# Performance work log

Measured on AMD Instinct MI355X. Metric: run time of the kernel, lower is better.

The kernel has to match this reference:

```python
import jax, jax.numpy as jnp
import numpy as np

NUM_CLASSES = 80
STRIDES = (8, 16, 32)
INPUT_SIZE = 640
DIST_THRESH_SQ = 64.0 * 64.0  # assignment uses euclidean dist < 64; compare squared


def make_anchors(input_size):
    pts = []
    for s in STRIDES:
        n = input_size // s
        yv, xv = np.meshgrid(np.arange(n), np.arange(n), indexing='ij')
        g = np.stack([xv, yv], -1).reshape(-1, 2).astype(np.float32) * s + s // 2
        pts.append(g)
    return jnp.asarray(np.concatenate(pts, 0))  # [A, 2]


def bce_logits(x, t):
    # BCEWithLogits, elementwise: -(t*log_sigmoid(x) + (1-t)*log_sigmoid(-x))
    return -(t * jax.nn.log_sigmoid(x) + (1.0 - t) * jax.nn.log_sigmoid(-x))


def iou_loss(pred_boxes, target_boxes):
    # pred: (cx, cy, log_w, log_h); target: (cx, cy, w, h) in pixels
    pc = pred_boxes[:, :2]
    ps = jnp.exp(pred_boxes[:, 2:4])
    p1 = pc - ps / 2.0
    p2 = pc + ps / 2.0
    t1 = target_boxes[:, :2] - target_boxes[:, 2:4] / 2.0
    t2 = target_boxes[:, :2] + target_boxes[:, 2:4] / 2.0
    i1 = jnp.maximum(p1, t1)
    i2 = jnp.minimum(p2, t2)
    inter = jnp.clip(i2[:, 0] - i1[:, 0], 0.0) * jnp.clip(i2[:, 1] - i1[:, 1], 0.0)
    pa = (p2[:, 0] - p1[:, 0]) * (p2[:, 1] - p1[:, 1])
    ta = (t2[:, 0] - t1[:, 0]) * (t2[:, 1] - t1[:, 1])
    union = pa + ta - inter
    return 1.0 - inter / (union + 1e-06)


def setup_inputs() -> dict:
    key = jax.random.key(0)
    k1, k2, k3, k4, k5 = jax.random.split(key, 5)
    B, M = 64, 50
    A = sum((INPUT_SIZE // s) ** 2 for s in STRIDES)  # 8400
    predictions = jax.random.normal(k1, (B, A, 5 + NUM_CLASSES), dtype=jnp.float32)
    cls = jax.random.randint(k2, (B, M), 0, NUM_CLASSES).astype(jnp.float32)
    valid = jax.random.uniform(k3, (B, M)) < 0.6
    cls = jnp.where(valid, cls, -1.0)
    centers = jax.random.uniform(k4, (B, M, 2), minval=0.05, maxval=0.95)
    wh = jax.random.uniform(k5, (B, M, 2), minval=0.02, maxval=0.3)
    targets = jnp.concatenate([cls[..., None], centers, wh], axis=-1).astype(jnp.float32)
    return {"predictions": predictions, "targets": targets, "input_size": 640}


def _per_image(pred, tgt, anchors, num_classes, input_size):
    # pred: [A, 5+C], tgt: [M, 5]
    valid = tgt[:, 0] >= 0.0                              # [M]
    gt_cls = tgt[:, 0].astype(jnp.int32)                  # [M]
    gt_boxes = tgt[:, 1:5] * input_size                   # [M, 4] pixels
    diff = gt_boxes[:, None, :2] - anchors[None, :, :]    # [M, A, 2]
    d2 = jnp.sum(diff * diff, axis=-1)                    # [M, A] squared dist
    d2 = jnp.where(valid[:, None], d2, jnp.inf)
    matched = jnp.argmin(d2, axis=0)                      # [A]
    min_d2 = jnp.min(d2, axis=0)                          # [A]
    pos = min_d2 < DIST_THRESH_SQ                         # [A]
    posf = pos.astype(pred.dtype)
    num_pos = posf.sum()

    obj_loss = bce_logits(pred[:, 4], posf).mean()

    cls_t = jax.nn.one_hot(gt_cls[matched], num_classes, dtype=pred.dtype)  # [A, C]
    cls_bce = bce_logits(pred[:, 5:], cls_t)                                # [A, C]
    denom = jnp.maximum(num_pos, 1.0)
    cls_loss = jnp.where(num_pos > 0,
                         (cls_bce * posf[:, None]).sum() / (denom * num_classes), 0.0)

    iou_l = iou_loss(pred[:, :4], gt_boxes[matched])      # [A]
    box_loss = jnp.where(num_pos > 0, (iou_l * posf).sum() / denom, 0.0)
    return obj_loss, cls_loss, box_loss, num_pos


def reference(predictions, targets, input_size):
    anchors = make_anchors(int(input_size))               # [A, 2]
    fsize = jnp.float32(input_size)
    obj, cls, box, npos = jax.vmap(
        lambda p, t: _per_image(p, t, anchors, NUM_CLASSES, fsize)
    )(predictions, targets)
    obj_loss = obj.sum()
    cls_loss = cls.sum()
    box_loss = box.sum()
    num_fg = npos.sum()
    total = 5.0 * box_loss + obj_loss + cls_loss
    return total, box_loss, obj_loss, cls_loss, num_fg
```

## Files before the change

kernel.cpp:

```cpp
#include <hip/hip_runtime.h>
#include <math.h>

#define NUM_CLASSES 80
#define MT 50
#define ATOT 8400
#define CH 85
#define BLOCK 256
#define CHUNK 256
#define NBY 33

__device__ __forceinline__ float softplus_fast(float x) {
    return fmaxf(x, 0.0f) + __logf(1.0f + __expf(-fabsf(x)));
}

__global__ void zero_acc_kernel(float* acc, int n) {
    int i = blockIdx.x * blockDim.x + threadIdx.x;
    if (i < n) acc[i] = 0.0f;
}

__global__ __launch_bounds__(BLOCK) void yolox_fused(
        const float* __restrict__ pred,
        const float* __restrict__ tgt,
        const int*   __restrict__ isz,
        float* __restrict__ acc) {
    const int b  = blockIdx.y;
    const int by = blockIdx.x;
    const int a0 = by * CHUNK;
    const int nanch = min(CHUNK, ATOT - a0);

    __shared__ float  raw[MT * 5];
    __shared__ float2 sxy[MT];
    __shared__ float2 swh[MT];
    __shared__ float  scls[MT];
    __shared__ int    snv;
    __shared__ int    smask[CHUNK];

    for (int i = threadIdx.x; i < MT * 5; i += BLOCK)
        raw[i] = tgt[(size_t)b * MT * 5 + i];
    __syncthreads();
    if (threadIdx.x == 0) {
        const float fsize = (float)(*isz);
        int nv = 0;
        for (int m = 0; m < MT; ++m) {
            const float c = raw[m * 5 + 0];
            if (c >= 0.0f) {
                sxy[nv]  = make_float2(raw[m * 5 + 1] * fsize, raw[m * 5 + 2] * fsize);
                swh[nv]  = make_float2(raw[m * 5 + 3] * fsize, raw[m * 5 + 4] * fsize);
                scls[nv] = c;
                ++nv;
            }
        }
        snv = nv;
    }
    __syncthreads();
    const int nv = snv;

    float box_s = 0.f, np_s = 0.f;
    smask[threadIdx.x] = -1;

    const int a = a0 + threadIdx.x;
    if (threadIdx.x < nanch) {
        int s, n, idx;
        if (a < 6400)      { s = 8;  n = 80; idx = a; }
        else if (a < 8000) { s = 16; n = 40; idx = a - 6400; }
        else               { s = 32; n = 20; idx = a - 8000; }
        const int yy = idx / n;
        const int xx = idx - yy * n;
        const float ax = (float)(xx * s + (s >> 1));
        const float ay = (float)(yy * s + (s >> 1));

        float best = INFINITY;
        int bestm = 0;
        for (int m = 0; m < nv; ++m) {
            const float2 g = sxy[m];
            const float dx = g.x - ax, dy = g.y - ay;
            const float d2 = dx * dx + dy * dy;
            if (d2 < best) { best = d2; bestm = m; }
        }
        const bool pos = best < 4096.0f;

        if (pos) {
            smask[threadIdx.x] = (int)scls[bestm];
            np_s = 1.0f;
            const float* p = pred + ((size_t)b * ATOT + (size_t)a) * CH;
            const float pcx = p[0], pcy = p[1];
            const float pw = __expf(p[2]), ph = __expf(p[3]);
            const float2 g  = sxy[bestm];
            const float2 wh = swh[bestm];
            const float p1x = pcx - pw * 0.5f, p2x = pcx + pw * 0.5f;
            const float p1y = pcy - ph * 0.5f, p2y = pcy + ph * 0.5f;
            const float t1x = g.x - wh.x * 0.5f, t2x = g.x + wh.x * 0.5f;
            const float t1y = g.y - wh.y * 0.5f, t2y = g.y + wh.y * 0.5f;
            const float iw = fminf(p2x, t2x) - fmaxf(p1x, t1x);
            const float ih = fminf(p2y, t2y) - fmaxf(p1y, t1y);
            const float inter = fmaxf(iw, 0.f) * fmaxf(ih, 0.f);
            const float pa = (p2x - p1x) * (p2y - p1y);
            const float ta = (t2x - t1x) * (t2y - t1y);
            const float uni = pa + ta - inter;
            box_s = 1.0f - inter / (uni + 1e-6f);
        }
    }
    __syncthreads();

    float obj_s = 0.f, cls_s = 0.f;
    const float* base = pred + ((size_t)b * ATOT + (size_t)a0) * CH;
    const int ngroups = (nanch * CH) >> 2;

    for (int g = threadIdx.x; g < ngroups; g += BLOCK) {
        const int le0 = g << 2;
        const unsigned la = __umulhi((unsigned)le0, 3233857729u) >> 6;
        const int c0 = le0 - (int)la * CH;
        const int m0 = smask[la];
        const bool need = (c0 >= 1 && c0 <= 4) || (m0 >= 0 && c0 >= 2);
        if (need) {
            const float4 x4 = *(const float4*)(base + le0);
            const float xs[4] = {x4.x, x4.y, x4.z, x4.w};
            #pragma unroll
            for (int j = 0; j < 4; ++j) {
                const int c = c0 + j;
                if (c == 4) {
                    obj_s += softplus_fast(xs[j]) - (m0 >= 0 ? xs[j] : 0.0f);
                } else if (c >= 5 && c < CH && m0 >= 0) {
                    cls_s += softplus_fast(xs[j]);
                    if (c - 5 == m0) cls_s -= xs[j];
                }
            }
        }
    }

    float v0 = obj_s, v1 = cls_s, v2 = box_s, v3 = np_s;
    for (int off = 32; off > 0; off >>= 1) {
        v0 += __shfl_down(v0, off, 64);
        v1 += __shfl_down(v1, off, 64);
        v2 += __shfl_down(v2, off, 64);
        v3 += __shfl_down(v3, off, 64);
    }
    __shared__ float sred[BLOCK / 64][4];
    const int wave = threadIdx.x >> 6;
    const int lane = threadIdx.x & 63;
    if (lane == 0) {
        sred[wave][0] = v0; sred[wave][1] = v1;
        sred[wave][2] = v2; sred[wave][3] = v3;
    }
    __syncthreads();
    if (threadIdx.x == 0) {
        float t0 = 0.f, t1 = 0.f, t2 = 0.f, t3 = 0.f;
        #pragma unroll
        for (int w = 0; w < BLOCK / 64; ++w) {
            t0 += sred[w][0]; t1 += sred[w][1];
            t2 += sred[w][2]; t3 += sred[w][3];
        }
        atomicAdd(&acc[b * 4 + 0], t0);
        atomicAdd(&acc[b * 4 + 1], t1);
        atomicAdd(&acc[b * 4 + 2], t2);
        atomicAdd(&acc[b * 4 + 3], t3);
    }
}

__global__ void yolox_stage2(const float* __restrict__ acc,
                             float* __restrict__ out, int B) {
    float obj = 0.f, cls = 0.f, box = 0.f, np = 0.f;
    for (int b = threadIdx.x; b < B; b += 64) {
        const float os = acc[b * 4 + 0];
        const float cs = acc[b * 4 + 1];
        const float bs = acc[b * 4 + 2];
        const float ps = acc[b * 4 + 3];
        obj += os * (1.0f / (float)ATOT);
        const float denom = fmaxf(ps, 1.0f);
        cls += (ps > 0.f) ? cs / (denom * (float)NUM_CLASSES) : 0.f;
        box += (ps > 0.f) ? bs / denom : 0.f;
        np  += ps;
    }
    for (int off = 32; off > 0; off >>= 1) {
        obj += __shfl_down(obj, off, 64);
        cls += __shfl_down(cls, off, 64);
        box += __shfl_down(box, off, 64);
        np  += __shfl_down(np,  off, 64);
    }
    if (threadIdx.x == 0) {
        out[0] = 5.0f * box + obj + cls;
        out[1] = box;
        out[2] = obj;
        out[3] = cls;
        out[4] = np;
    }
}

extern "C" void kernel_launch(void* const* d_in, const int* in_sizes, int n_in,
                              void* d_out, int out_size, void* d_ws, size_t ws_size,
                              hipStream_t stream) {
    const float* pred = (const float*)d_in[0];
    const float* tgt  = (const float*)d_in[1];
    const int*   isz  = (const int*)d_in[2];
    float* out = (float*)d_out;
    float* acc = (float*)d_ws;

    const int B = in_sizes[1] / (MT * 5);

    zero_acc_kernel<<<1, BLOCK, 0, stream>>>(acc, B * 4);

    dim3 grid(NBY, B);
    yolox_fused<<<grid, BLOCK, 0, stream>>>(pred, tgt, isz, acc);

    yolox_stage2<<<1, 64, 0, stream>>>(acc, out, B);
}
```

Before: 285.3 us.

## Replace atomics with per-block partial slots, parallelize target compaction via ballot

Drops the zero-init kernel and the atomics by having each block write its partial sums to its own workspace slot, which the second stage then reduces. Target compaction now uses a wavefront ballot and popcount instead of a single serial thread. The matched-class logit term is read directly per positive anchor rather than through a class mask, and the streaming loop gets an unroll hint. This removes one kernel launch and some serialized setup, in exchange for a larger workspace and a heavier stage-2 reduction.

```diff
diff --git a/kernel.cpp b/kernel.cpp
--- a/kernel.cpp
+++ b/kernel.cpp
@@ -11,11 +11,6 @@
 
 __device__ __forceinline__ float softplus_fast(float x) {
     return fmaxf(x, 0.0f) + __logf(1.0f + __expf(-fabsf(x)));
-}
-
-__global__ void zero_acc_kernel(float* acc, int n) {
-    int i = blockIdx.x * blockDim.x + threadIdx.x;
-    if (i < n) acc[i] = 0.0f;
 }
 
 __global__ __launch_bounds__(BLOCK) void yolox_fused(
@@ -28,46 +23,44 @@
     const int a0 = by * CHUNK;
     const int nanch = min(CHUNK, ATOT - a0);
 
-    __shared__ float  raw[MT * 5];
-    __shared__ float2 sxy[MT];
-    __shared__ float2 swh[MT];
-    __shared__ float  scls[MT];
+    __shared__ float2 sxy[64];
+    __shared__ float2 swh[64];
+    __shared__ float  scls[64];
     __shared__ int    snv;
-    __shared__ int    smask[CHUNK];
-
-    for (int i = threadIdx.x; i < MT * 5; i += BLOCK)
-        raw[i] = tgt[(size_t)b * MT * 5 + i];
-    __syncthreads();
-    if (threadIdx.x == 0) {
+    __shared__ float  sposf[CHUNK];
+
+    if (threadIdx.x < 64) {
+        const int m = threadIdx.x;
         const float fsize = (float)(*isz);
-        int nv = 0;
-        for (int m = 0; m < MT; ++m) {
-            const float c = raw[m * 5 + 0];
-            if (c >= 0.0f) {
-                sxy[nv]  = make_float2(raw[m * 5 + 1] * fsize, raw[m * 5 + 2] * fsize);
-                swh[nv]  = make_float2(raw[m * 5 + 3] * fsize, raw[m * 5 + 4] * fsize);
-                scls[nv] = c;
-                ++nv;
-            }
-        }
-        snv = nv;
-    }
+        float c = -1.0f, x = 0.f, y = 0.f, w = 0.f, h = 0.f;
+        if (m < MT) {
+            const float* tb = tgt + (size_t)b * MT * 5 + (size_t)m * 5;
+            c = tb[0];
+            x = tb[1] * fsize; y = tb[2] * fsize;
+            w = tb[3] * fsize; h = tb[4] * fsize;
+        }
+        const bool valid = (m < MT) && (c >= 0.0f);
+        const unsigned long long ballot = __ballot(valid);
+        const int slot = __popcll(ballot & ((1ull << threadIdx.x) - 1ull));
+        if (valid) {
+            sxy[slot]  = make_float2(x, y);
+            swh[slot]  = make_float2(w, h);
+            scls[slot] = c;
+        }
+        if (m == 0) snv = (int)__popcll(ballot);
+    }
+    sposf[threadIdx.x] = 0.0f;
     __syncthreads();
     const int nv = snv;
 
-    float box_s = 0.f, np_s = 0.f;
-    smask[threadIdx.x] = -1;
+    float box_s = 0.f, np_s = 0.f, cls_s = 0.f, obj_s = 0.f;
 
     const int a = a0 + threadIdx.x;
     if (threadIdx.x < nanch) {
-        int s, n, idx;
-        if (a < 6400)      { s = 8;  n = 80; idx = a; }
-        else if (a < 8000) { s = 16; n = 40; idx = a - 6400; }
-        else               { s = 32; n = 20; idx = a - 8000; }
-        const int yy = idx / n;
-        const int xx = idx - yy * n;
-        const float ax = (float)(xx * s + (s >> 1));
-        const float ay = (float)(yy * s + (s >> 1));
+        float ax, ay;
+        if (a < 6400)      { const int yy = a / 80;              const int xx = a - yy * 80;  ax = (float)(xx * 8  + 4);  ay = (float)(yy * 8  + 4); }
+        else if (a < 8000) { const int i2 = a - 6400; const int yy = i2 / 40; const int xx = i2 - yy * 40; ax = (float)(xx * 16 + 8);  ay = (float)(yy * 16 + 8); }
+        else               { const int i2 = a - 8000; const int yy = i2 / 20; const int xx = i2 - yy * 20; ax = (float)(xx * 32 + 16); ay = (float)(yy * 32 + 16); }
 
         float best = INFINITY;
         int bestm = 0;
@@ -80,9 +73,12 @@
         const bool pos = best < 4096.0f;
 
         if (pos) {
-            smask[threadIdx.x] = (int)scls[bestm];
+            sposf[threadIdx.x] = 1.0f;
             np_s = 1.0f;
             const float* p = pred + ((size_t)b * ATOT + (size_t)a) * CH;
+            const int gcls = (int)scls[bestm];
+            cls_s = -p[5 + gcls];
+
             const float pcx = p[0], pcy = p[1];
             const float pw = __expf(p[2]), ph = __expf(p[3]);
             const float2 g  = sxy[bestm];
@@ -102,16 +98,17 @@
     }
     __syncthreads();
 
-    float obj_s = 0.f, cls_s = 0.f;
     const float* base = pred + ((size_t)b * ATOT + (size_t)a0) * CH;
     const int ngroups = (nanch * CH) >> 2;
 
+    #pragma unroll 4
     for (int g = threadIdx.x; g < ngroups; g += BLOCK) {
         const int le0 = g << 2;
         const unsigned la = __umulhi((unsigned)le0, 3233857729u) >> 6;
         const int c0 = le0 - (int)la * CH;
-        const int m0 = smask[la];
-        const bool need = (c0 >= 1 && c0 <= 4) || (m0 >= 0 && c0 >= 2);
+        const float posf = sposf[la];
+        const bool mpos = posf > 0.0f;
+        const bool need = (c0 >= 1 && c0 <= 4) || (mpos && c0 >= 2);
         if (need) {
             const float4 x4 = *(const float4*)(base + le0);
             const float xs[4] = {x4.x, x4.y, x4.z, x4.w};
@@ -119,10 +116,9 @@
             for (int j = 0; j < 4; ++j) {
                 const int c = c0 + j;
                 if (c == 4) {
-                    obj_s += softplus_fast(xs[j]) - (m0 >= 0 ? xs[j] : 0.0f);
-                } else if (c >= 5 && c < CH && m0 >= 0) {
+                    obj_s += softplus_fast(xs[j]) - posf * xs[j];
+                } else if (c >= 5 && c < CH && mpos) {
                     cls_s += softplus_fast(xs[j]);
-                    if (c - 5 == m0) cls_s -= xs[j];
                 }
             }
         }
@@ -150,39 +146,58 @@
             t0 += sred[w][0]; t1 += sred[w][1];
             t2 += sred[w][2]; t3 += sred[w][3];
         }
-        atomicAdd(&acc[b * 4 + 0], t0);
-        atomicAdd(&acc[b * 4 + 1], t1);
-        atomicAdd(&acc[b * 4 + 2], t2);
-        atomicAdd(&acc[b * 4 + 3], t3);
-    }
-}
-
-__global__ void yolox_stage2(const float* __restrict__ acc,
-                             float* __restrict__ out, int B) {
+        float* slot = acc + ((size_t)b * NBY + by) * 4;
+        slot[0] = t0; slot[1] = t1; slot[2] = t2; slot[3] = t3;
+    }
+}
+
+__global__ __launch_bounds__(BLOCK) void yolox_stage2(
+        const float* __restrict__ acc,
+        float* __restrict__ out, int B) {
     float obj = 0.f, cls = 0.f, box = 0.f, np = 0.f;
-    for (int b = threadIdx.x; b < B; b += 64) {
-        const float os = acc[b * 4 + 0];
-        const float cs = acc[b * 4 + 1];
-        const float bs = acc[b * 4 + 2];
-        const float ps = acc[b * 4 + 3];
+    for (int bb = threadIdx.x; bb < B; bb += BLOCK) {
+        float os = 0.f, cs = 0.f, bs = 0.f, ps = 0.f;
+        const float* s = acc + (size_t)bb * NBY * 4;
+        #pragma unroll
+        for (int j = 0; j < NBY; ++j) {
+            os += s[j * 4 + 0];
+            cs += s[j * 4 + 1];
+            bs += s[j * 4 + 2];
+            ps += s[j * 4 + 3];
+        }
         obj += os * (1.0f / (float)ATOT);
         const float denom = fmaxf(ps, 1.0f);
         cls += (ps > 0.f) ? cs / (denom * (float)NUM_CLASSES) : 0.f;
         box += (ps > 0.f) ? bs / denom : 0.f;
         np  += ps;
     }
+    float v0 = obj, v1 = cls, v2 = box, v3 = np;
     for (int off = 32; off > 0; off >>= 1) {
-        obj += __shfl_down(obj, off, 64);
-        cls += __shfl_down(cls, off, 64);
-        box += __shfl_down(box, off, 64);
-        np  += __shfl_down(np,  off, 64);
-    }
+        v0 += __shfl_down(v0, off, 64);
+        v1 += __shfl_down(v1, off, 64);
+        v2 += __shfl_down(v2, off, 64);
+        v3 += __shfl_down(v3, off, 64);
+    }
+    __shared__ float sred[BLOCK / 64][4];
+    const int wave = threadIdx.x >> 6;
+    const int lane = threadIdx.x & 63;
+    if (lane == 0) {
+        sred[wave][0] = v0; sred[wave][1] = v1;
+        sred[wave][2] = v2; sred[wave][3] = v3;
+    }
+    __syncthreads();
     if (threadIdx.x == 0) {
-        out[0] = 5.0f * box + obj + cls;
-        out[1] = box;
-        out[2] = obj;
-        out[3] = cls;
-        out[4] = np;
+        float t0 = 0.f, t1 = 0.f, t2 = 0.f, t3 = 0.f;
+        #pragma unroll
+        for (int w = 0; w < BLOCK / 64; ++w) {
+            t0 += sred[w][0]; t1 += sred[w][1];
+            t2 += sred[w][2]; t3 += sred[w][3];
+        }
+        out[0] = 5.0f * t2 + t0 + t1;
+        out[1] = t2;
+        out[2] = t0;
+        out[3] = t1;
+        out[4] = t3;
     }
 }
 
@@ -197,10 +212,7 @@
 
     const int B = in_sizes[1] / (MT * 5);
 
-    zero_acc_kernel<<<1, BLOCK, 0, stream>>>(acc, B * 4);
-
     dim3 grid(NBY, B);
     yolox_fused<<<grid, BLOCK, 0, stream>>>(pred, tgt, isz, acc);
-
-    yolox_stage2<<<1, 64, 0, stream>>>(acc, out, B);
-}
+    yolox_stage2<<<1, BLOCK, 0, stream>>>(acc, out, B);
+}
```

Result: faster. 276.8 us (-3.0%).
